# Performance work log

Hardware: AMD Instinct MI355X
Metric: run time of the kernel (lower is better)

Reference implementation:

```python
import jax, jax.numpy as jnp
import numpy as np

PRIOR_SCALE = 0.1
LOG_PS = float(np.log(PRIOR_SCALE))
NEG_SLOPE = 0.01  # nn.LeakyReLU default


def _kl_mean(mu, log_sigma, axes):
    # kl_div(mu_q, lsq, 0, lsp) = lsp - lsq + (exp(lsq)^2 + mu^2)/(2*exp(lsp)^2) - 0.5, mean over param dims
    kl = LOG_PS - log_sigma + (jnp.exp(log_sigma) ** 2 + mu ** 2) / (2.0 * PRIOR_SCALE ** 2) - 0.5
    return jnp.mean(kl, axis=axes)  # -> per-feature [F]


def _bayes_linear(x, wmu, wls, bmu, bls, ew, eb):
    # x: [B,F,Din], wmu/wls/ew: [F,Din,Dout], bmu/bls/eb: [F,Dout]
    W = wmu + jnp.exp(wls) * ew
    b = bmu + jnp.exp(bls) * eb
    out = jnp.einsum('bfi,fio->bfo', x, W) + b[None, :, :]
    kl_f = _kl_mean(wmu, wls, (1, 2)) + _kl_mean(bmu, bls, (1,))  # [F]
    return out, kl_f


def setup_inputs() -> dict:
    key = jax.random.key(0)
    ks = jax.random.split(key, 20)
    B, F, H = 16384, 64, 64
    inp = {
        'f': jax.random.normal(ks[0], (B, F), jnp.float32),
        'wmu0': jax.random.normal(ks[1], (F, 1, H), jnp.float32),
        'wls0': jax.random.normal(ks[2], (F, 1, H), jnp.float32),
        'bmu0': jax.random.normal(ks[3], (F, H), jnp.float32),
        'bls0': jax.random.normal(ks[4], (F, H), jnp.float32),
        'ew0': jax.random.normal(ks[5], (F, 1, H), jnp.float32),
        'eb0': jax.random.normal(ks[6], (F, H), jnp.float32),
        'wmu1': jax.random.normal(ks[7], (F, H, H), jnp.float32),
        'wls1': jax.random.normal(ks[8], (F, H, H), jnp.float32),
        'bmu1': jax.random.normal(ks[9], (F, H), jnp.float32),
        'bls1': jax.random.normal(ks[10], (F, H), jnp.float32),
        'ew1': jax.random.normal(ks[11], (F, H, H), jnp.float32),
        'eb1': jax.random.normal(ks[12], (F, H), jnp.float32),
        'wmu2': jax.random.normal(ks[13], (F, H, 1), jnp.float32),
        'wls2': jax.random.normal(ks[14], (F, H, 1), jnp.float32),
        'bmu2': jax.random.normal(ks[15], (F, 1), jnp.float32),
        'bls2': jax.random.normal(ks[16], (F, 1), jnp.float32),
        'ew2': jax.random.normal(ks[17], (F, H, 1), jnp.float32),
        'eb2': jax.random.normal(ks[18], (F, 1), jnp.float32),
        'bias': jnp.zeros((1,), jnp.float32),
    }
    return inp


def reference(f, wmu0, wls0, bmu0, bls0, ew0, eb0,
              wmu1, wls1, bmu1, bls1, ew1, eb1,
              wmu2, wls2, bmu2, bls2, ew2, eb2, bias):
    x = f[:, :, None]  # [B,F,1] (per-feature scalar input)
    out, kl0 = _bayes_linear(x, wmu0, wls0, bmu0, bls0, ew0, eb0)
    out = jax.nn.leaky_relu(out, NEG_SLOPE)
    out, kl1 = _bayes_linear(out, wmu1, wls1, bmu1, bls1, ew1, eb1)
    out = jax.nn.leaky_relu(out, NEG_SLOPE)  # dropout p=0 -> identity
    out, kl2 = _bayes_linear(out, wmu2, wls2, bmu2, bls2, ew2, eb2)  # [B,F,1]
    kl_total = jnp.sum(kl0 + kl1 + kl2)  # sum over features of per-feature kl sums
    conc = out[:, :, 0]  # concat of per-feature scalar outputs -> [B,F]
    y = jnp.sum(conc, axis=-1) + bias[0]  # feature_dropout p=0 -> identity
    return y, kl_total
```

## Files before the change

### kernel.cpp

```cpp
#include <hip/hip_runtime.h>
#include <hip/hip_fp16.h>

typedef _Float16 f16x8 __attribute__((ext_vector_type(8)));
typedef float floatx4 __attribute__((ext_vector_type(4)));

#define NEG 0.01f
#define KL_C (-2.8025850929940457f)

#define W0HOFF 131072
#define B0HOFF 133120
#define B1OFF  135168
#define W2OFF  139264
#define B2OFF  143360
#define KLPOFF 143424

__global__ void bayesnam_prep(const float* __restrict__ wmu0, const float* __restrict__ wls0,
                              const float* __restrict__ bmu0, const float* __restrict__ bls0,
                              const float* __restrict__ ew0,  const float* __restrict__ eb0,
                              const float* __restrict__ wmu1, const float* __restrict__ wls1,
                              const float* __restrict__ bmu1, const float* __restrict__ bls1,
                              const float* __restrict__ ew1,  const float* __restrict__ eb1,
                              const float* __restrict__ wmu2, const float* __restrict__ wls2,
                              const float* __restrict__ bmu2, const float* __restrict__ bls2,
                              const float* __restrict__ ew2,  const float* __restrict__ eb2,
                              const float* __restrict__ bias,
                              float* __restrict__ ws, float* __restrict__ out) {
    const int tid = threadIdx.x;
    const int bx  = blockIdx.x;
    __shared__ float red[256];
    if (bx < 256) {
        const int f = bx >> 2;
        const int q = bx & 3;
        __shared__ float w1s[16 * 65];
        const size_t base = (size_t)f * 4096 + (size_t)q * 1024;
        float klacc = 0.f;
        #pragma unroll
        for (int i = 0; i < 4; ++i) {
            const int idx = i * 256 + tid;
            const float m = wmu1[base + idx];
            const float l = wls1[base + idx];
            const float e = ew1[base + idx];
            const float ex = expf(l);
            w1s[(idx >> 6) * 65 + (idx & 63)] = fmaf(ex, e, m);
            klacc += (KL_C - l) + 50.f * fmaf(ex, ex, m * m);
        }
        red[tid] = klacc * 0.000244140625f;
        __syncthreads();
        for (int s = 128; s > 0; s >>= 1) {
            if (tid < s) red[tid] += red[tid + s];
            __syncthreads();
        }
        if (tid == 0) ws[KLPOFF + bx] = red[0];
        if (tid < 128) {
            const int n   = tid >> 5;
            const int ls  = tid & 31;
            const int s   = ls >> 4;
            const int l15 = ls & 15;
            const int lg  = 2 * (q & 1) + s;
            const int lane = lg * 16 + l15;
            const int kk  = q >> 1;
            const int col = n * 16 + l15;
            union { _Float16 h[8]; uint4 u; } fr;
            #pragma unroll
            for (int j = 0; j < 8; ++j) fr.h[j] = (_Float16)w1s[(8 * s + j) * 65 + col];
            ((uint4*)ws)[(size_t)f * 512 + kk * 256 + n * 64 + lane] = fr.u;
        }
    } else {
        float klacc = 0.f;
        _Float16* w0h = (_Float16*)(ws + W0HOFF);
        _Float16* b0h = (_Float16*)(ws + B0HOFF);
        for (int idx = (bx - 256) * 256 + tid; idx < 16448; idx += 2048) {
            const float *mu, *ls, *ew;
            int j, kind; float scale;
            if (idx < 4096)       { j = idx;         mu = wmu0; ls = wls0; ew = ew0; scale = 0.015625f; kind = 0; }
            else if (idx < 8192)  { j = idx - 4096;  mu = bmu0; ls = bls0; ew = eb0; scale = 0.015625f; kind = 1; }
            else if (idx < 12288) { j = idx - 8192;  mu = bmu1; ls = bls1; ew = eb1; scale = 0.015625f; kind = 2; }
            else if (idx < 16384) { j = idx - 12288; mu = wmu2; ls = wls2; ew = ew2; scale = 0.015625f; kind = 3; }
            else                  { j = idx - 16384; mu = bmu2; ls = bls2; ew = eb2; scale = 1.0f;      kind = 4; }
            const float m = mu[j], l = ls[j], e = ew[j];
            const float ex = expf(l);
            const float w  = fmaf(ex, e, m);
            if (kind == 0)      w0h[j] = (_Float16)w;
            else if (kind == 1) b0h[j] = (_Float16)w;
            else if (kind == 2) ws[B1OFF + j] = w;
            else if (kind == 3) ws[W2OFF + j] = w;
            else                ws[B2OFF + j] = w;
            klacc += scale * ((KL_C - l) + 50.f * fmaf(ex, ex, m * m));
        }
        const float bv = bias[0];
        for (int i = (bx - 256) * 256 + tid; i < 16384; i += 2048) out[i] = bv;
        red[tid] = klacc;
        __syncthreads();
        for (int s = 128; s > 0; s >>= 1) {
            if (tid < s) red[tid] += red[tid + s];
            __syncthreads();
        }
        if (tid == 0) ws[KLPOFF + 256 + (bx - 256)] = red[0];
    }
}

__global__ __launch_bounds__(256, 4) void bayesnam_main(const float* __restrict__ fin,
                                                        const float* __restrict__ ws,
                                                        float* __restrict__ out) {
    __shared__ uint4 fragLDS[2048];
    const int tid = threadIdx.x;
    const int l   = tid & 63;
    const int wid = tid >> 6;
    const int l15 = l & 15;
    const int lg  = l >> 4;
    const int rowbase = blockIdx.x * 128 + wid * 32;
    const int f0 = blockIdx.y * 4;

    {
        const char* gsrc = (const char*)ws + (size_t)f0 * 8192;
        #pragma unroll
        for (int i = 0; i < 8; ++i) {
            const int chunk = (wid * 8 + i) * 1024;
            __builtin_amdgcn_global_load_lds(
                (const __attribute__((address_space(1))) unsigned int*)(gsrc + chunk + l * 16),
                (__attribute__((address_space(3))) unsigned int*)((char*)fragLDS + chunk),
                16, 0, 0);
        }
    }

    if (blockIdx.x == 0 && blockIdx.y == 0 && tid < 64) {
        float k = 0.f;
        #pragma unroll
        for (int i = 0; i < 5; ++i) {
            const int p = tid + i * 64;
            if (p < 264) k += ws[KLPOFF + p];
        }
        k += __shfl_xor(k, 32, 64); k += __shfl_xor(k, 16, 64); k += __shfl_xor(k, 8, 64);
        k += __shfl_xor(k, 4, 64);  k += __shfl_xor(k, 2, 64);  k += __shfl_xor(k, 1, 64);
        if (tid == 0) out[16384] = k;
    }

    const _Float16* __restrict__ w0h = (const _Float16*)(ws + W0HOFF);
    const _Float16* __restrict__ b0h = (const _Float16*)(ws + B0HOFF);
    const _Float16 negh = (_Float16)0.01f;

    const floatx4 x0v = *(const floatx4*)(fin + (size_t)(rowbase + l15) * 64 + f0);
    const floatx4 x1v = *(const floatx4*)(fin + (size_t)(rowbase + 16 + l15) * 64 + f0);

    __syncthreads();

    float yacc[2][4];
    #pragma unroll
    for (int r = 0; r < 2; ++r)
        #pragma unroll
        for (int q = 0; q < 4; ++q) yacc[r][q] = 0.f;
    float b2sum = 0.f;

    #pragma unroll 1
    for (int fi = 0; fi < 4; ++fi) {
        const int f = f0 + fi;
        const float* b1p = ws + B1OFF + f * 64;
        const float* w2p = ws + W2OFF + f * 64;
        const _Float16 x0h = (_Float16)x0v[fi];
        const _Float16 x1h = (_Float16)x1v[fi];

        floatx4 acc[2][4];
        #pragma unroll
        for (int n = 0; n < 4; ++n) {
            const float bv = b1p[n * 16 + l15];
            acc[0][n] = floatx4{bv, bv, bv, bv};
            acc[1][n] = floatx4{bv, bv, bv, bv};
        }

        #pragma unroll
        for (int kk = 0; kk < 2; ++kk) {
            const int kb = kk * 32 + lg * 8;
            union HU { uint4 u; f16x8 v; };
            HU wu, bu;
            wu.u = *(const uint4*)(w0h + f * 64 + kb);
            bu.u = *(const uint4*)(b0h + f * 64 + kb);

            f16x8 t0 = wu.v * x0h + bu.v;
            f16x8 a0 = __builtin_elementwise_max(t0, t0 * negh);
            f16x8 t1 = wu.v * x1h + bu.v;
            f16x8 a1 = __builtin_elementwise_max(t1, t1 * negh);

            const uint4* bp = fragLDS + ((fi * 8 + kk * 4) * 64 + l);
            #pragma unroll
            for (int n = 0; n < 4; ++n) {
                HU bf; bf.u = bp[n * 64];
                acc[0][n] = __builtin_amdgcn_mfma_f32_16x16x32_f16(a0, bf.v, acc[0][n], 0, 0, 0);
                acc[1][n] = __builtin_amdgcn_mfma_f32_16x16x32_f16(a1, bf.v, acc[1][n], 0, 0, 0);
            }
        }

        #pragma unroll
        for (int n = 0; n < 4; ++n) {
            const float w2v = w2p[n * 16 + l15];
            #pragma unroll
            for (int r = 0; r < 2; ++r)
                #pragma unroll
                for (int q = 0; q < 4; ++q) {
                    float v = acc[r][n][q];
                    v = fmaxf(v, NEG * v);
                    yacc[r][q] = fmaf(v, w2v, yacc[r][q]);
                }
        }
        b2sum += ws[B2OFF + f];
    }

    #pragma unroll
    for (int r = 0; r < 2; ++r)
        #pragma unroll
        for (int q = 0; q < 4; ++q) {
            float v = yacc[r][q];
            v += __shfl_xor(v, 1, 64);
            v += __shfl_xor(v, 2, 64);
            v += __shfl_xor(v, 4, 64);
            v += __shfl_xor(v, 8, 64);
            yacc[r][q] = v;
        }
    if (l15 == 0) {
        #pragma unroll
        for (int r = 0; r < 2; ++r)
            #pragma unroll
            for (int q = 0; q < 4; ++q)
                atomicAdd(&out[rowbase + r * 16 + lg * 4 + q], yacc[r][q] + b2sum);
    }
}

extern "C" void kernel_launch(void* const* d_in, const int* in_sizes, int n_in,
                              void* d_out, int out_size, void* d_ws, size_t ws_size,
                              hipStream_t stream) {
    const float* fin  = (const float*)d_in[0];
    const float* wmu0 = (const float*)d_in[1];
    const float* wls0 = (const float*)d_in[2];
    const float* bmu0 = (const float*)d_in[3];
    const float* bls0 = (const float*)d_in[4];
    const float* ew0  = (const float*)d_in[5];
    const float* eb0  = (const float*)d_in[6];
    const float* wmu1 = (const float*)d_in[7];
    const float* wls1 = (const float*)d_in[8];
    const float* bmu1 = (const float*)d_in[9];
    const float* bls1 = (const float*)d_in[10];
    const float* ew1  = (const float*)d_in[11];
    const float* eb1  = (const float*)d_in[12];
    const float* wmu2 = (const float*)d_in[13];
    const float* wls2 = (const float*)d_in[14];
    const float* bmu2 = (const float*)d_in[15];
    const float* bls2 = (const float*)d_in[16];
    const float* ew2  = (const float*)d_in[17];
    const float* eb2  = (const float*)d_in[18];
    const float* bias = (const float*)d_in[19];

    float* ws  = (float*)d_ws;
    float* out = (float*)d_out;

    hipLaunchKernelGGL(bayesnam_prep, dim3(264), dim3(256), 0, stream,
                       wmu0, wls0, bmu0, bls0, ew0, eb0,
                       wmu1, wls1, bmu1, bls1, ew1, eb1,
                       wmu2, wls2, bmu2, bls2, ew2, eb2,
                       bias, ws, out);

    hipLaunchKernelGGL(bayesnam_main, dim3(128, 16), dim3(256), 0, stream,
                       fin, ws, out);
}
```

Baseline: 30.83 us.

## Halve features per block, pack layer-2 epilogue in fp16, raise occupancy

Each main-kernel block now handles 2 features instead of 4, so the grid doubles to 128x32, the LDS fragment buffer halves, and launch bounds ask for 8 waves per SIMD. The hidden layer is processed in two halves with fewer live accumulators. The last-layer weights are stored as fp16 in a permuted layout so the leaky-ReLU and dot product run as packed half2 math. This cuts register and LDS pressure to allow more resident blocks, but doubles the atomicAdds to the output, doubles redundant layer-0 work per row, and accumulates the final reduction in fp16, which risks precision loss.

```diff
diff --git a/kernel.cpp b/kernel.cpp
--- a/kernel.cpp
+++ b/kernel.cpp
@@ -2,7 +2,10 @@
 #include <hip/hip_fp16.h>
 
 typedef _Float16 f16x8 __attribute__((ext_vector_type(8)));
+typedef _Float16 f16x2 __attribute__((ext_vector_type(2)));
+typedef __fp16   fp16v2 __attribute__((ext_vector_type(2)));
 typedef float floatx4 __attribute__((ext_vector_type(4)));
+typedef float floatx2 __attribute__((ext_vector_type(2)));
 
 #define NEG 0.01f
 #define KL_C (-2.8025850929940457f)
@@ -10,9 +13,15 @@
 #define W0HOFF 131072
 #define B0HOFF 133120
 #define B1OFF  135168
-#define W2OFF  139264
+#define W2HOFF 139264
 #define B2OFF  143360
 #define KLPOFF 143424
+
+__device__ __forceinline__ f16x2 cvt2(float a, float b) {
+    union { fp16v2 p; f16x2 h; } u;
+    u.p = __builtin_amdgcn_cvt_pkrtz(a, b);
+    return u.h;
+}
 
 __global__ void bayesnam_prep(const float* __restrict__ wmu0, const float* __restrict__ wls0,
                               const float* __restrict__ bmu0, const float* __restrict__ bls0,
@@ -69,6 +78,7 @@
         float klacc = 0.f;
         _Float16* w0h = (_Float16*)(ws + W0HOFF);
         _Float16* b0h = (_Float16*)(ws + B0HOFF);
+        _Float16* w2h = (_Float16*)(ws + W2HOFF);
         for (int idx = (bx - 256) * 256 + tid; idx < 16448; idx += 2048) {
             const float *mu, *ls, *ew;
             int j, kind; float scale;
@@ -83,7 +93,10 @@
             if (kind == 0)      w0h[j] = (_Float16)w;
             else if (kind == 1) b0h[j] = (_Float16)w;
             else if (kind == 2) ws[B1OFF + j] = w;
-            else if (kind == 3) ws[W2OFF + j] = w;
+            else if (kind == 3) {
+                const int h = j & 63;
+                w2h[(j & ~63) | ((h >> 5) << 5) | ((h & 15) << 1) | ((h >> 4) & 1)] = (_Float16)w;
+            }
             else                ws[B2OFF + j] = w;
             klacc += scale * ((KL_C - l) + 50.f * fmaf(ex, ex, m * m));
         }
@@ -99,23 +112,23 @@
     }
 }
 
-__global__ __launch_bounds__(256, 4) void bayesnam_main(const float* __restrict__ fin,
+__global__ __launch_bounds__(256, 8) void bayesnam_main(const float* __restrict__ fin,
                                                         const float* __restrict__ ws,
                                                         float* __restrict__ out) {
-    __shared__ uint4 fragLDS[2048];
+    __shared__ uint4 fragLDS[1024];
     const int tid = threadIdx.x;
     const int l   = tid & 63;
     const int wid = tid >> 6;
     const int l15 = l & 15;
     const int lg  = l >> 4;
     const int rowbase = blockIdx.x * 128 + wid * 32;
-    const int f0 = blockIdx.y * 4;
+    const int f0 = blockIdx.y * 2;
 
     {
         const char* gsrc = (const char*)ws + (size_t)f0 * 8192;
         #pragma unroll
-        for (int i = 0; i < 8; ++i) {
-            const int chunk = (wid * 8 + i) * 1024;
+        for (int i = 0; i < 4; ++i) {
+            const int chunk = (wid * 4 + i) * 1024;
             __builtin_amdgcn_global_load_lds(
                 (const __attribute__((address_space(1))) unsigned int*)(gsrc + chunk + l * 16),
                 (__attribute__((address_space(3))) unsigned int*)((char*)fragLDS + chunk),
@@ -137,68 +150,70 @@
 
     const _Float16* __restrict__ w0h = (const _Float16*)(ws + W0HOFF);
     const _Float16* __restrict__ b0h = (const _Float16*)(ws + B0HOFF);
+    const _Float16* __restrict__ w2h = (const _Float16*)(ws + W2HOFF);
     const _Float16 negh = (_Float16)0.01f;
-
-    const floatx4 x0v = *(const floatx4*)(fin + (size_t)(rowbase + l15) * 64 + f0);
-    const floatx4 x1v = *(const floatx4*)(fin + (size_t)(rowbase + 16 + l15) * 64 + f0);
+    const f16x2 neg2 = {(_Float16)0.01f, (_Float16)0.01f};
+
+    const floatx2 x0v = *(const floatx2*)(fin + (size_t)(rowbase + l15) * 64 + f0);
+    const floatx2 x1v = *(const floatx2*)(fin + (size_t)(rowbase + 16 + l15) * 64 + f0);
 
     __syncthreads();
 
-    float yacc[2][4];
+    f16x2 ypk[2][4];
     #pragma unroll
     for (int r = 0; r < 2; ++r)
         #pragma unroll
-        for (int q = 0; q < 4; ++q) yacc[r][q] = 0.f;
+        for (int q = 0; q < 4; ++q) ypk[r][q] = f16x2{(_Float16)0.f, (_Float16)0.f};
     float b2sum = 0.f;
 
     #pragma unroll 1
-    for (int fi = 0; fi < 4; ++fi) {
+    for (int fi = 0; fi < 2; ++fi) {
         const int f = f0 + fi;
-        const float* b1p = ws + B1OFF + f * 64;
-        const float* w2p = ws + W2OFF + f * 64;
         const _Float16 x0h = (_Float16)x0v[fi];
         const _Float16 x1h = (_Float16)x1v[fi];
 
-        floatx4 acc[2][4];
-        #pragma unroll
-        for (int n = 0; n < 4; ++n) {
-            const float bv = b1p[n * 16 + l15];
-            acc[0][n] = floatx4{bv, bv, bv, bv};
-            acc[1][n] = floatx4{bv, bv, bv, bv};
-        }
-
+        f16x8 a0[2], a1[2];
         #pragma unroll
         for (int kk = 0; kk < 2; ++kk) {
             const int kb = kk * 32 + lg * 8;
-            union HU { uint4 u; f16x8 v; };
-            HU wu, bu;
+            union HU { uint4 u; f16x8 v; } wu, bu;
             wu.u = *(const uint4*)(w0h + f * 64 + kb);
             bu.u = *(const uint4*)(b0h + f * 64 + kb);
-
             f16x8 t0 = wu.v * x0h + bu.v;
-            f16x8 a0 = __builtin_elementwise_max(t0, t0 * negh);
+            a0[kk] = __builtin_elementwise_max(t0, t0 * negh);
             f16x8 t1 = wu.v * x1h + bu.v;
-            f16x8 a1 = __builtin_elementwise_max(t1, t1 * negh);
-
-            const uint4* bp = fragLDS + ((fi * 8 + kk * 4) * 64 + l);
-            #pragma unroll
-            for (int n = 0; n < 4; ++n) {
-                HU bf; bf.u = bp[n * 64];
-                acc[0][n] = __builtin_amdgcn_mfma_f32_16x16x32_f16(a0, bf.v, acc[0][n], 0, 0, 0);
-                acc[1][n] = __builtin_amdgcn_mfma_f32_16x16x32_f16(a1, bf.v, acc[1][n], 0, 0, 0);
+            a1[kk] = __builtin_elementwise_max(t1, t1 * negh);
+        }
+
+        const float* b1p = ws + B1OFF + f * 64;
+        #pragma unroll 1
+        for (int nh = 0; nh < 2; ++nh) {
+            floatx4 acc[2][2];
+            #pragma unroll
+            for (int n2 = 0; n2 < 2; ++n2) {
+                const float bv = b1p[(nh * 2 + n2) * 16 + l15];
+                acc[0][n2] = floatx4{bv, bv, bv, bv};
+                acc[1][n2] = floatx4{bv, bv, bv, bv};
             }
-        }
-
-        #pragma unroll
-        for (int n = 0; n < 4; ++n) {
-            const float w2v = w2p[n * 16 + l15];
+            #pragma unroll
+            for (int kk = 0; kk < 2; ++kk) {
+                #pragma unroll
+                for (int n2 = 0; n2 < 2; ++n2) {
+                    union HU { uint4 u; f16x8 v; } bf;
+                    bf.u = fragLDS[fi * 512 + kk * 256 + (nh * 2 + n2) * 64 + l];
+                    acc[0][n2] = __builtin_amdgcn_mfma_f32_16x16x32_f16(a0[kk], bf.v, acc[0][n2], 0, 0, 0);
+                    acc[1][n2] = __builtin_amdgcn_mfma_f32_16x16x32_f16(a1[kk], bf.v, acc[1][n2], 0, 0, 0);
+                }
+            }
+            const f16x2 w2pair = *(const f16x2*)(w2h + f * 64 + nh * 32 + l15 * 2);
             #pragma unroll
             for (int r = 0; r < 2; ++r)
                 #pragma unroll
                 for (int q = 0; q < 4; ++q) {
-                    float v = acc[r][n][q];
-                    v = fmaxf(v, NEG * v);
-                    yacc[r][q] = fmaf(v, w2v, yacc[r][q]);
+                    f16x2 h2 = (r == 0) ? cvt2(acc[0][0][q], acc[0][1][q])
+                                        : cvt2(acc[1][0][q], acc[1][1][q]);
+                    f16x2 lk = __builtin_elementwise_max(h2, h2 * neg2);
+                    ypk[r][q] = lk * w2pair + ypk[r][q];
                 }
         }
         b2sum += ws[B2OFF + f];
@@ -208,20 +223,14 @@
     for (int r = 0; r < 2; ++r)
         #pragma unroll
         for (int q = 0; q < 4; ++q) {
-            float v = yacc[r][q];
+            float v = (float)ypk[r][q][0] + (float)ypk[r][q][1];
             v += __shfl_xor(v, 1, 64);
             v += __shfl_xor(v, 2, 64);
             v += __shfl_xor(v, 4, 64);
             v += __shfl_xor(v, 8, 64);
-            yacc[r][q] = v;
-        }
-    if (l15 == 0) {
-        #pragma unroll
-        for (int r = 0; r < 2; ++r)
-            #pragma unroll
-            for (int q = 0; q < 4; ++q)
-                atomicAdd(&out[rowbase + r * 16 + lg * 4 + q], yacc[r][q] + b2sum);
-    }
+            if (l15 == 0)
+                atomicAdd(&out[rowbase + r * 16 + lg * 4 + q], v + b2sum);
+        }
 }
 
 extern "C" void kernel_launch(void* const* d_in, const int* in_sizes, int n_in,
@@ -257,6 +266,6 @@
                        wmu2, wls2, bmu2, bls2, ew2, eb2,
                        bias, ws, out);
 
-    hipLaunchKernelGGL(bayesnam_main, dim3(128, 16), dim3(256), 0, stream,
+    hipLaunchKernelGGL(bayesnam_main, dim3(128, 32), dim3(256), 0, stream,
                        fin, ws, out);
 }
```

Result: slower. 33.49 us (+8.6%).

## Pack layer-2 epilogue into fp16x2 math and split prep across more blocks

Applied to the files above, without the earlier changes.

The layer-2 epilogue now converts pairs of MFMA accumulators to packed fp16, applies leaky ReLU and FMAs against fp16 output weights that prep stores pre-permuted, which roughly halves the VALU work per element. The prep kernel splits each feature's W1 into eight blocks instead of four, for more parallelism and a smaller LDS transpose. The feature loop is unrolled by two. Accumulating the per-row output in fp16 costs accuracy and risks exceeding the tolerance.

```diff
diff --git a/kernel.cpp b/kernel.cpp
--- a/kernel.cpp
+++ b/kernel.cpp
@@ -2,6 +2,8 @@
 #include <hip/hip_fp16.h>
 
 typedef _Float16 f16x8 __attribute__((ext_vector_type(8)));
+typedef _Float16 f16x2 __attribute__((ext_vector_type(2)));
+typedef __fp16   fp16v2 __attribute__((ext_vector_type(2)));
 typedef float floatx4 __attribute__((ext_vector_type(4)));
 
 #define NEG 0.01f
@@ -10,9 +12,15 @@
 #define W0HOFF 131072
 #define B0HOFF 133120
 #define B1OFF  135168
-#define W2OFF  139264
+#define W2HOFF 139264
 #define B2OFF  143360
 #define KLPOFF 143424
+
+__device__ __forceinline__ f16x2 cvt2(float a, float b) {
+    union { fp16v2 p; f16x2 h; } u;
+    u.p = __builtin_amdgcn_cvt_pkrtz(a, b);
+    return u.h;
+}
 
 __global__ void bayesnam_prep(const float* __restrict__ wmu0, const float* __restrict__ wls0,
                               const float* __restrict__ bmu0, const float* __restrict__ bls0,
@@ -28,14 +36,14 @@
     const int tid = threadIdx.x;
     const int bx  = blockIdx.x;
     __shared__ float red[256];
-    if (bx < 256) {
-        const int f = bx >> 2;
-        const int q = bx & 3;
-        __shared__ float w1s[16 * 65];
-        const size_t base = (size_t)f * 4096 + (size_t)q * 1024;
+    if (bx < 512) {
+        const int f = bx >> 3;
+        const int g = bx & 7;
+        __shared__ float w1s[8 * 65];
+        const size_t base = (size_t)f * 4096 + (size_t)g * 512;
         float klacc = 0.f;
         #pragma unroll
-        for (int i = 0; i < 4; ++i) {
+        for (int i = 0; i < 2; ++i) {
             const int idx = i * 256 + tid;
             const float m = wmu1[base + idx];
             const float l = wls1[base + idx];
@@ -51,25 +59,23 @@
             __syncthreads();
         }
         if (tid == 0) ws[KLPOFF + bx] = red[0];
-        if (tid < 128) {
-            const int n   = tid >> 5;
-            const int ls  = tid & 31;
-            const int s   = ls >> 4;
-            const int l15 = ls & 15;
-            const int lg  = 2 * (q & 1) + s;
-            const int lane = lg * 16 + l15;
-            const int kk  = q >> 1;
+        if (tid < 64) {
+            const int n   = tid >> 4;
+            const int l15 = tid & 15;
+            const int kk  = g >> 2;
+            const int lg  = g & 3;
             const int col = n * 16 + l15;
             union { _Float16 h[8]; uint4 u; } fr;
             #pragma unroll
-            for (int j = 0; j < 8; ++j) fr.h[j] = (_Float16)w1s[(8 * s + j) * 65 + col];
-            ((uint4*)ws)[(size_t)f * 512 + kk * 256 + n * 64 + lane] = fr.u;
+            for (int j = 0; j < 8; ++j) fr.h[j] = (_Float16)w1s[j * 65 + col];
+            ((uint4*)ws)[(size_t)f * 512 + kk * 256 + n * 64 + lg * 16 + l15] = fr.u;
         }
     } else {
         float klacc = 0.f;
         _Float16* w0h = (_Float16*)(ws + W0HOFF);
         _Float16* b0h = (_Float16*)(ws + B0HOFF);
-        for (int idx = (bx - 256) * 256 + tid; idx < 16448; idx += 2048) {
+        _Float16* w2h = (_Float16*)(ws + W2HOFF);
+        for (int idx = (bx - 512) * 256 + tid; idx < 16448; idx += 2048) {
             const float *mu, *ls, *ew;
             int j, kind; float scale;
             if (idx < 4096)       { j = idx;         mu = wmu0; ls = wls0; ew = ew0; scale = 0.015625f; kind = 0; }
@@ -83,19 +89,22 @@
             if (kind == 0)      w0h[j] = (_Float16)w;
             else if (kind == 1) b0h[j] = (_Float16)w;
             else if (kind == 2) ws[B1OFF + j] = w;
-            else if (kind == 3) ws[W2OFF + j] = w;
+            else if (kind == 3) {
+                const int h = j & 63;
+                w2h[(j & ~63) | ((h >> 5) << 5) | ((h & 15) << 1) | ((h >> 4) & 1)] = (_Float16)w;
+            }
             else                ws[B2OFF + j] = w;
             klacc += scale * ((KL_C - l) + 50.f * fmaf(ex, ex, m * m));
         }
         const float bv = bias[0];
-        for (int i = (bx - 256) * 256 + tid; i < 16384; i += 2048) out[i] = bv;
+        for (int i = (bx - 512) * 256 + tid; i < 16384; i += 2048) out[i] = bv;
         red[tid] = klacc;
         __syncthreads();
         for (int s = 128; s > 0; s >>= 1) {
             if (tid < s) red[tid] += red[tid + s];
             __syncthreads();
         }
-        if (tid == 0) ws[KLPOFF + 256 + (bx - 256)] = red[0];
+        if (tid == 0) ws[KLPOFF + 512 + (bx - 512)] = red[0];
     }
 }
 
@@ -126,9 +135,9 @@
     if (blockIdx.x == 0 && blockIdx.y == 0 && tid < 64) {
         float k = 0.f;
         #pragma unroll
-        for (int i = 0; i < 5; ++i) {
+        for (int i = 0; i < 9; ++i) {
             const int p = tid + i * 64;
-            if (p < 264) k += ws[KLPOFF + p];
+            if (p < 520) k += ws[KLPOFF + p];
         }
         k += __shfl_xor(k, 32, 64); k += __shfl_xor(k, 16, 64); k += __shfl_xor(k, 8, 64);
         k += __shfl_xor(k, 4, 64);  k += __shfl_xor(k, 2, 64);  k += __shfl_xor(k, 1, 64);
@@ -137,70 +146,71 @@
 
     const _Float16* __restrict__ w0h = (const _Float16*)(ws + W0HOFF);
     const _Float16* __restrict__ b0h = (const _Float16*)(ws + B0HOFF);
-    const _Float16 negh = (_Float16)0.01f;
+    const _Float16* __restrict__ w2h = (const _Float16*)(ws + W2HOFF);
+    const f16x2 neg2 = {(_Float16)0.01f, (_Float16)0.01f};
 
     const floatx4 x0v = *(const floatx4*)(fin + (size_t)(rowbase + l15) * 64 + f0);
     const floatx4 x1v = *(const floatx4*)(fin + (size_t)(rowbase + 16 + l15) * 64 + f0);
 
     __syncthreads();
 
-    float yacc[2][4];
+    f16x2 ypk[2][4];
     #pragma unroll
     for (int r = 0; r < 2; ++r)
         #pragma unroll
-        for (int q = 0; q < 4; ++q) yacc[r][q] = 0.f;
+        for (int q = 0; q < 4; ++q) ypk[r][q] = f16x2{(_Float16)0.f, (_Float16)0.f};
     float b2sum = 0.f;
 
-    #pragma unroll 1
+    #pragma unroll 2
     for (int fi = 0; fi < 4; ++fi) {
         const int f = f0 + fi;
-        const float* b1p = ws + B1OFF + f * 64;
-        const float* w2p = ws + W2OFF + f * 64;
         const _Float16 x0h = (_Float16)x0v[fi];
         const _Float16 x1h = (_Float16)x1v[fi];
 
         floatx4 acc[2][4];
-        #pragma unroll
-        for (int n = 0; n < 4; ++n) {
-            const float bv = b1p[n * 16 + l15];
-            acc[0][n] = floatx4{bv, bv, bv, bv};
-            acc[1][n] = floatx4{bv, bv, bv, bv};
+        {
+            const float* b1p = ws + B1OFF + f * 64;
+            #pragma unroll
+            for (int n = 0; n < 4; ++n) {
+                const float bv = b1p[n * 16 + l15];
+                acc[0][n] = floatx4{bv, bv, bv, bv};
+                acc[1][n] = floatx4{bv, bv, bv, bv};
+            }
         }
 
         #pragma unroll
         for (int kk = 0; kk < 2; ++kk) {
             const int kb = kk * 32 + lg * 8;
-            union HU { uint4 u; f16x8 v; };
-            HU wu, bu;
+            union HU { uint4 u; f16x8 v; } wu, bu;
             wu.u = *(const uint4*)(w0h + f * 64 + kb);
             bu.u = *(const uint4*)(b0h + f * 64 + kb);
-
             f16x8 t0 = wu.v * x0h + bu.v;
-            f16x8 a0 = __builtin_elementwise_max(t0, t0 * negh);
+            f16x8 a0 = __builtin_elementwise_max(t0, t0 * neg2[0]);
             f16x8 t1 = wu.v * x1h + bu.v;
-            f16x8 a1 = __builtin_elementwise_max(t1, t1 * negh);
-
-            const uint4* bp = fragLDS + ((fi * 8 + kk * 4) * 64 + l);
+            f16x8 a1 = __builtin_elementwise_max(t1, t1 * neg2[0]);
+
             #pragma unroll
             for (int n = 0; n < 4; ++n) {
-                HU bf; bf.u = bp[n * 64];
+                union HU2 { uint4 u; f16x8 v; } bf;
+                bf.u = fragLDS[(fi * 8 + kk * 4 + n) * 64 + l];
                 acc[0][n] = __builtin_amdgcn_mfma_f32_16x16x32_f16(a0, bf.v, acc[0][n], 0, 0, 0);
                 acc[1][n] = __builtin_amdgcn_mfma_f32_16x16x32_f16(a1, bf.v, acc[1][n], 0, 0, 0);
             }
         }
 
-        #pragma unroll
-        for (int n = 0; n < 4; ++n) {
-            const float w2v = w2p[n * 16 + l15];
-            #pragma unroll
-            for (int r = 0; r < 2; ++r)
-                #pragma unroll
-                for (int q = 0; q < 4; ++q) {
-                    float v = acc[r][n][q];
-                    v = fmaxf(v, NEG * v);
-                    yacc[r][q] = fmaf(v, w2v, yacc[r][q]);
-                }
-        }
+        const f16x2 w2p0 = *(const f16x2*)(w2h + f * 64 + l15 * 2);
+        const f16x2 w2p1 = *(const f16x2*)(w2h + f * 64 + 32 + l15 * 2);
+        #pragma unroll
+        for (int r = 0; r < 2; ++r)
+            #pragma unroll
+            for (int q = 0; q < 4; ++q) {
+                f16x2 h0 = cvt2(acc[r][0][q], acc[r][1][q]);
+                f16x2 h1 = cvt2(acc[r][2][q], acc[r][3][q]);
+                f16x2 lk0 = __builtin_elementwise_max(h0, h0 * neg2);
+                f16x2 lk1 = __builtin_elementwise_max(h1, h1 * neg2);
+                ypk[r][q] = lk0 * w2p0 + ypk[r][q];
+                ypk[r][q] = lk1 * w2p1 + ypk[r][q];
+            }
         b2sum += ws[B2OFF + f];
     }
 
@@ -208,20 +218,14 @@
     for (int r = 0; r < 2; ++r)
         #pragma unroll
         for (int q = 0; q < 4; ++q) {
-            float v = yacc[r][q];
+            float v = (float)ypk[r][q][0] + (float)ypk[r][q][1];
             v += __shfl_xor(v, 1, 64);
             v += __shfl_xor(v, 2, 64);
             v += __shfl_xor(v, 4, 64);
             v += __shfl_xor(v, 8, 64);
-            yacc[r][q] = v;
-        }
-    if (l15 == 0) {
-        #pragma unroll
-        for (int r = 0; r < 2; ++r)
-            #pragma unroll
-            for (int q = 0; q < 4; ++q)
-                atomicAdd(&out[rowbase + r * 16 + lg * 4 + q], yacc[r][q] + b2sum);
-    }
+            if (l15 == 0)
+                atomicAdd(&out[rowbase + r * 16 + lg * 4 + q], v + b2sum);
+        }
 }
 
 extern "C" void kernel_launch(void* const* d_in, const int* in_sizes, int n_in,
@@ -251,7 +255,7 @@
     float* ws  = (float*)d_ws;
     float* out = (float*)d_out;
 
-    hipLaunchKernelGGL(bayesnam_prep, dim3(264), dim3(256), 0, stream,
+    hipLaunchKernelGGL(bayesnam_prep, dim3(520), dim3(256), 0, stream,
                        wmu0, wls0, bmu0, bls0, ew0, eb0,
                        wmu1, wls1, bmu1, bls1, ew1, eb1,
                        wmu2, wls2, bmu2, bls2, ew2, eb2,
```

New measurement: 29.30 us. 1.05x faster.
